# Optimization experiments

Measured on AMD Instinct MI355X. Metric: run time of the kernel, lower is better.

The kernel has to match this reference:

```python
import jax, jax.numpy as jnp
import numpy as np

EPS = 1e-5  # BatchNorm eps (torch default)

def setup_inputs() -> dict:
    key = jax.random.key(0)
    ks = jax.random.split(key, 24)
    B, NX, NY, F = 8, 128, 128, 128
    dims = [2 * F, 512, 256, 128, 64]
    d = {
        'x': jax.random.normal(ks[0], (B, NX, F), dtype=jnp.float32),
        'y': jax.random.normal(ks[1], (B, NY, F), dtype=jnp.float32),
    }
    i = 2
    for li, (din, dout) in enumerate(zip(dims[:-1], dims[1:]), start=1):
        d[f'w{li}'] = jax.random.normal(ks[i], (dout, din), dtype=jnp.float32) * (1.0 / np.sqrt(din)); i += 1
        d[f'b{li}'] = jax.random.normal(ks[i], (dout,), dtype=jnp.float32) * 0.02; i += 1
        if li < 4:  # BatchNorm1d on hidden layers only (eval mode: running stats)
            d[f'g{li}'] = 1.0 + 0.1 * jax.random.normal(ks[i], (dout,), dtype=jnp.float32); i += 1
            d[f'be{li}'] = 0.1 * jax.random.normal(ks[i], (dout,), dtype=jnp.float32); i += 1
            d[f'm{li}'] = 0.1 * jax.random.normal(ks[i], (dout,), dtype=jnp.float32); i += 1
            d[f'v{li}'] = 0.5 + jax.random.uniform(ks[i], (dout,), dtype=jnp.float32); i += 1
    return d

def _bn(h, g, be, m, v):
    # BatchNorm1d in eval mode over the channel (last) axis
    return (h - m) * (g * jax.lax.rsqrt(v + EPS)) + be

def reference(x, y,
              w1, b1, g1, be1, m1, v1,
              w2, b2, g2, be2, m2, v2,
              w3, b3, g3, be3, m3, v3,
              w4, b4):
    F = x.shape[-1]
    # First Linear on cat([x_i, y_j]) == split-weight broadcast add: avoids the
    # (B,nx,ny,2F) pairwise concat the torch code materializes (same math).
    wx, wy = w1[:, :F], w1[:, F:]                      # (512,F) each
    hx = jnp.einsum('bif,hf->bih', x, wx)              # (B,nx,512)
    hy = jnp.einsum('bjf,hf->bjh', y, wy)              # (B,ny,512)
    h = hx[:, :, None, :] + hy[:, None, :, :] + b1     # (B,nx,ny,512)
    h = jax.nn.relu(_bn(h, g1, be1, m1, v1))           # dropout is identity in eval
    h = jax.nn.relu(_bn(jnp.einsum('bijh,oh->bijo', h, w2) + b2, g2, be2, m2, v2))
    h = jax.nn.relu(_bn(jnp.einsum('bijh,oh->bijo', h, w3) + b3, g3, be3, m3, v3))
    e = jnp.einsum('bijh,oh->bijo', h, w4) + b4        # (B,nx,ny,64) embeddings
    # PSD path: einsum('bijk,bilk->bijl', e, e).sum(-1)
    #         == sum_k e[b,i,j,k] * (sum_l e[b,i,l,k])  -- avoids (B,nx,ny,ny)
    s = e.sum(axis=2)                                  # (B,nx,64)
    kernel = jnp.einsum('bijk,bik->bij', e, s)         # (B,nx,ny)
    return kernel
```

## Files before the change

### kernel.cpp

```cpp
#include <hip/hip_runtime.h>

#define EPS 1e-5f

typedef _Float16 half8 __attribute__((ext_vector_type(8)));
typedef _Float16 half4 __attribute__((ext_vector_type(4)));
typedef float f32x16 __attribute__((ext_vector_type(16)));
typedef float f32x4v __attribute__((ext_vector_type(4)));


__global__ __launch_bounds__(256)
void pre_kernel(
    const float* __restrict__ x, const float* __restrict__ y,
    const float* __restrict__ w1, const float* __restrict__ b1,
    const float* __restrict__ g1, const float* __restrict__ be1,
    const float* __restrict__ m1, const float* __restrict__ v1,
    const float* __restrict__ w2, const float* __restrict__ b2,
    const float* __restrict__ g2, const float* __restrict__ be2,
    const float* __restrict__ m2, const float* __restrict__ v2,
    const float* __restrict__ w3, const float* __restrict__ b3,
    const float* __restrict__ g3, const float* __restrict__ be3,
    const float* __restrict__ m3, const float* __restrict__ v3,
    const float* __restrict__ w4,
    _Float16* __restrict__ hxh, _Float16* __restrict__ hyh,
    _Float16* __restrict__ w2h, _Float16* __restrict__ w3h,
    _Float16* __restrict__ w4h,
    float* __restrict__ b2f, float* __restrict__ b3f)
{
    const int t = threadIdx.x;

    if (blockIdx.x >= 256) {
        int tid = (blockIdx.x - 256) * 256 + t;
        const int nth = 64 * 256;
        for (int idx = tid; idx < 256 * 512; idx += nth) {
            int n = idx >> 9, k = idx & 511;
            float a = g2[n] * rsqrtf(v2[n] + EPS);
            int addr = ((n >> 5) * 32 + (k >> 4)) * 512 + ((k >> 3) & 1) * 256 + (n & 31) * 8 + (k & 7);
            w2h[addr] = (_Float16)(a * w2[idx]);
        }
        for (int idx = tid; idx < 128 * 256; idx += nth) {
            int n = idx >> 8, k = idx & 255;
            float a = g3[n] * rsqrtf(v3[n] + EPS);
            int addr = ((n >> 5) * 16 + (k >> 4)) * 512 + ((k >> 3) & 1) * 256 + (n & 31) * 8 + (k & 7);
            w3h[addr] = (_Float16)(a * w3[idx]);
        }
        for (int idx = tid; idx < 64 * 128; idx += nth) {
            int n = idx >> 7, k = idx & 127;
            int addr = ((n >> 5) * 8 + (k >> 4)) * 512 + ((k >> 3) & 1) * 256 + (n & 31) * 8 + (k & 7);
            w4h[addr] = (_Float16)w4[idx];
        }
        if (tid < 256) {
            float a = g2[tid] * rsqrtf(v2[tid] + EPS);
            b2f[tid] = a * b2[tid] + be2[tid] - m2[tid] * a;
        } else if (tid < 384) {
            int n = tid - 256;
            float a = g3[n] * rsqrtf(v3[n] + EPS);
            b3f[n] = a * b3[n] + be3[n] - m3[n] * a;
        }
        return;
    }

    const int rg = blockIdx.x & 31;
    const int ng = (blockIdx.x >> 5) & 3;
    const int which = blockIdx.x >> 7;

    constexpr int LDA = 136;
    __shared__ _Float16 sh[32 * 136 + 128 * 136] __attribute__((aligned(16)));
    _Float16* xa = sh;
    _Float16* wb = sh + 32 * 136;

    const int rowbase = rg * 32;
    const float* src = which ? y : x;

#pragma unroll
    for (int p = 0; p < 4; ++p) {
        int c = p * 256 + t;
        int r = c >> 5, fo = (c & 31) * 4;
        f32x4v v = *(const f32x4v*)(src + (size_t)(rowbase + r) * 128 + fo);
        half4 h; h[0] = (_Float16)v[0]; h[1] = (_Float16)v[1];
        h[2] = (_Float16)v[2]; h[3] = (_Float16)v[3];
        *(half4*)(xa + r * LDA + fo) = h;
    }
#pragma unroll
    for (int p = 0; p < 16; ++p) {
        int c = p * 256 + t;
        int n = c >> 5, fo = (c & 31) * 4;
        f32x4v v = *(const f32x4v*)(w1 + (size_t)(ng * 128 + n) * 256 + which * 128 + fo);
        half4 h; h[0] = (_Float16)v[0]; h[1] = (_Float16)v[1];
        h[2] = (_Float16)v[2]; h[3] = (_Float16)v[3];
        *(half4*)(wb + n * LDA + fo) = h;
    }
    __syncthreads();

    const int wid = t >> 6;
    const int l = t & 63;
    const int l31 = l & 31, lh = l >> 5;

    f32x16 acc = (f32x16)0.f;
#pragma unroll
    for (int kc = 0; kc < 8; ++kc) {
        half8 af = *(const half8*)(xa + l31 * LDA + kc * 16 + lh * 8);
        half8 bf = *(const half8*)(wb + (wid * 32 + l31) * LDA + kc * 16 + lh * 8);
        acc = __builtin_amdgcn_mfma_f32_32x32x16_f16(af, bf, acc, 0, 0, 0);
    }

    const int n = ng * 128 + wid * 32 + l31;
    float alpha = g1[n] * rsqrtf(v1[n] + EPS);
    if (which == 0) {
        float bias = alpha * b1[n] + be1[n] - m1[n] * alpha;
#pragma unroll
        for (int r = 0; r < 16; ++r) {
            int m = (r & 3) + 8 * (r >> 2) + 4 * lh;
            hxh[(size_t)(rowbase + m) * 512 + n] = (_Float16)(alpha * acc[r] + bias);
        }
    } else {
        const int ks = n >> 4, lhh = (n >> 3) & 1, c = n & 7;
#pragma unroll
        for (int r = 0; r < 16; ++r) {
            int m = (r & 3) + 8 * (r >> 2) + 4 * lh;
            int R = rowbase + m;
            int bb = R >> 7, j = R & 127;
            int addr = bb * 65536 + ((j >> 5) * 32 + ks) * 512 + lhh * 256 + (j & 31) * 8 + c;
            hyh[addr] = (_Float16)(alpha * acc[r]);
        }
    }
}

__global__ __launch_bounds__(1024, 4)
void fused_kernel(
    const _Float16* __restrict__ hxh, const _Float16* __restrict__ hyh,
    const _Float16* __restrict__ w2h, const _Float16* __restrict__ w3h,
    const _Float16* __restrict__ w4h,
    const float* __restrict__ b2f, const float* __restrict__ b3f,
    const float* __restrict__ b4,
    float* __restrict__ out)
{
    constexpr int LD2 = 264;
    constexpr int LD3 = 136;
    constexpr int LDE = 68;

    __shared__ char smem[6400 + 67584] __attribute__((aligned(16)));
    _Float16* hxs = (_Float16*)smem;
    float* spart  = (float*)(smem + 2048);
    float* ss     = (float*)(smem + 6144);
    char* R1 = smem + 6400;
    _Float16* a2  = (_Float16*)R1;
    _Float16* a3  = (_Float16*)R1;
    float*    es  = (float*)R1;

    const int b  = blockIdx.x >> 6;
    const int ip = blockIdx.x & 63;
    const int i0 = ip * 2;
    const int t = threadIdx.x;
    const int wid = t >> 6;
    const int l   = t & 63;
    const int l31 = l & 31;
    const int lh  = l >> 5;

    if (t < 128) {
        int iv = t >> 6;
        *(half8*)(hxs + iv * 512 + (t & 63) * 8) =
            *(const half8*)(hxh + (size_t)(b * 128 + i0 + iv) * 512 + (t & 63) * 8);
    }
    __syncthreads();

    const int wm = wid >> 2, wn = wid & 3;

    const _Float16* pa  = hyh + (size_t)b * 65536 + (size_t)(wm * 32) * 512 + l * 8;
    const _Float16* pb0 = w2h + (size_t)(2 * wn) * 32 * 512 + l * 8;
    const _Float16* pb1 = pb0 + 32 * 512;

    const float bb0 = b2f[wn * 64 + l31];
    const float bb1 = b2f[wn * 64 + 32 + l31];
    f32x16 d0 = (f32x16)bb0, d1 = (f32x16)bb1;
    f32x16 e0 = (f32x16)bb0, e1 = (f32x16)bb1;

    half8 A0, B00, B01;
    half8 A1, B10, B11;

    auto LD0 = [&](int ks) {
        A0  = *(const half8*)(pa  + (size_t)ks * 512);
        B00 = *(const half8*)(pb0 + (size_t)ks * 512);
        B01 = *(const half8*)(pb1 + (size_t)ks * 512);
    };
    auto LD1 = [&](int ks) {
        A1  = *(const half8*)(pa  + (size_t)ks * 512);
        B10 = *(const half8*)(pb0 + (size_t)ks * 512);
        B11 = *(const half8*)(pb1 + (size_t)ks * 512);
    };
    auto RELU = [&](half8 a, half8 rx) {
        half8 s = a + rx;
        half8 af;
#pragma unroll
        for (int c = 0; c < 8; ++c)
            af[c] = s[c] > (_Float16)0.f ? s[c] : (_Float16)0.f;
        return af;
    };
    auto STEP0 = [&](int ks) {
        half8 rx0 = *(const half8*)(hxs + ks * 16 + lh * 8);
        half8 rx1 = *(const half8*)(hxs + 512 + ks * 16 + lh * 8);
        half8 af = RELU(A0, rx0);
        d0 = __builtin_amdgcn_mfma_f32_32x32x16_f16(af, B00, d0, 0, 0, 0);
        d1 = __builtin_amdgcn_mfma_f32_32x32x16_f16(af, B01, d1, 0, 0, 0);
        af = RELU(A0, rx1);
        e0 = __builtin_amdgcn_mfma_f32_32x32x16_f16(af, B00, e0, 0, 0, 0);
        e1 = __builtin_amdgcn_mfma_f32_32x32x16_f16(af, B01, e1, 0, 0, 0);
    };
    auto STEP1 = [&](int ks) {
        half8 rx0 = *(const half8*)(hxs + ks * 16 + lh * 8);
        half8 rx1 = *(const half8*)(hxs + 512 + ks * 16 + lh * 8);
        half8 af = RELU(A1, rx0);
        d0 = __builtin_amdgcn_mfma_f32_32x32x16_f16(af, B10, d0, 0, 0, 0);
        d1 = __builtin_amdgcn_mfma_f32_32x32x16_f16(af, B11, d1, 0, 0, 0);
        af = RELU(A1, rx1);
        e0 = __builtin_amdgcn_mfma_f32_32x32x16_f16(af, B10, e0, 0, 0, 0);
        e1 = __builtin_amdgcn_mfma_f32_32x32x16_f16(af, B11, e1, 0, 0, 0);
    };

    LD0(0);
#pragma unroll 2
    for (int ks = 0; ks < 32; ks += 2) {
        if (ks + 1 < 32) LD1(ks + 1);
        STEP0(ks);
        if (ks + 2 < 32) LD0(ks + 2);
        if (ks + 1 < 32) STEP1(ks + 1);
    }

    auto TAIL = [&](const f32x16& c0, const f32x16& c1, int iv) {
#pragma unroll
        for (int r = 0; r < 16; ++r) {
            int m = wm * 32 + (r & 3) + 8 * (r >> 2) + 4 * lh;
            a2[m * LD2 + wn * 64 + l31]      = (_Float16)fmaxf(c0[r], 0.f);
            a2[m * LD2 + wn * 64 + 32 + l31] = (_Float16)fmaxf(c1[r], 0.f);
        }
        __syncthreads();

        f32x16 g = (f32x16)(b3f[wn * 32 + l31]);
#pragma unroll 4
        for (int kc = 0; kc < 16; ++kc) {
            half8 bfr = *(const half8*)(w3h + (wn * 16 + kc) * 512 + l * 8);
            half8 af  = *(const half8*)(a2 + (wm * 32 + l31) * LD2 + kc * 16 + lh * 8);
            g = __builtin_amdgcn_mfma_f32_32x32x16_f16(af, bfr, g, 0, 0, 0);
        }
        __syncthreads();
#pragma unroll
        for (int r = 0; r < 16; ++r) {
            int m = wm * 32 + (r & 3) + 8 * (r >> 2) + 4 * lh;
            a3[m * LD3 + wn * 32 + l31] = (_Float16)fmaxf(g[r], 0.f);
        }
        __syncthreads();

        f32x16 acc4;
        const int wm4 = wid >> 1, wn4 = wid & 1;
        if (wid < 8) {
            acc4 = (f32x16)(b4[wn4 * 32 + l31]);
#pragma unroll
            for (int kc = 0; kc < 8; ++kc) {
                half8 afr = *(const half8*)(a3 + (wm4 * 32 + l31) * LD3 + kc * 16 + lh * 8);
                half8 bfr = *(const half8*)(w4h + (wn4 * 8 + kc) * 512 + l * 8);
                acc4 = __builtin_amdgcn_mfma_f32_32x32x16_f16(afr, bfr, acc4, 0, 0, 0);
            }
        }
        __syncthreads();
        if (wid < 8) {
#pragma unroll
            for (int r = 0; r < 16; ++r) {
                int m = wm4 * 32 + (r & 3) + 8 * (r >> 2) + 4 * lh;
                es[m * LDE + wn4 * 32 + l31] = acc4[r];
            }
        }
        __syncthreads();

        {
            float sv = 0.f;
#pragma unroll
            for (int jj = 0; jj < 8; ++jj) sv += es[(wid + jj * 16) * LDE + l];
            spart[wid * 64 + l] = sv;
        }
        __syncthreads();
        if (t < 64) {
            float s2 = 0.f;
#pragma unroll
            for (int r = 0; r < 16; ++r) s2 += spart[r * 64 + t];
            ss[t] = s2;
        }
        __syncthreads();
        {
            const int j = t >> 3, q = t & 7;
            float p = 0.f;
#pragma unroll
            for (int c = 0; c < 8; ++c) {
                int k = q + 8 * c;
                p += es[j * LDE + k] * ss[k];
            }
            p += __shfl_xor(p, 1);
            p += __shfl_xor(p, 2);
            p += __shfl_xor(p, 4);
            if (q == 0) out[(size_t)(b * 128 + iv) * 128 + j] = p;
        }
        __syncthreads();
    };

    TAIL(d0, d1, i0);
    TAIL(e0, e1, i0 + 1);
}

extern "C" void kernel_launch(void* const* d_in, const int* in_sizes, int n_in,
                              void* d_out, int out_size, void* d_ws, size_t ws_size,
                              hipStream_t stream)
{
    (void)in_sizes; (void)n_in; (void)out_size; (void)ws_size;

    const float* x   = (const float*)d_in[0];
    const float* y   = (const float*)d_in[1];
    const float* w1  = (const float*)d_in[2];
    const float* b1  = (const float*)d_in[3];
    const float* g1  = (const float*)d_in[4];
    const float* be1 = (const float*)d_in[5];
    const float* m1  = (const float*)d_in[6];
    const float* v1  = (const float*)d_in[7];
    const float* w2  = (const float*)d_in[8];
    const float* b2  = (const float*)d_in[9];
    const float* g2  = (const float*)d_in[10];
    const float* be2 = (const float*)d_in[11];
    const float* m2  = (const float*)d_in[12];
    const float* v2  = (const float*)d_in[13];
    const float* w3  = (const float*)d_in[14];
    const float* b3  = (const float*)d_in[15];
    const float* g3  = (const float*)d_in[16];
    const float* be3 = (const float*)d_in[17];
    const float* m3  = (const float*)d_in[18];
    const float* v3  = (const float*)d_in[19];
    const float* w4  = (const float*)d_in[20];
    const float* b4  = (const float*)d_in[21];
    float* out = (float*)d_out;

    float* b2f = (float*)d_ws;
    float* b3f = b2f + 256;
    _Float16* w2h = (_Float16*)(b3f + 128);
    _Float16* w3h = w2h + 131072;
    _Float16* w4h = w3h + 32768;
    _Float16* hxh = w4h + 8192;
    _Float16* hyh = hxh + 524288;

    hipLaunchKernelGGL(pre_kernel, dim3(320), dim3(256), 0, stream,
                       x, y, w1, b1, g1, be1, m1, v1,
                       w2, b2, g2, be2, m2, v2,
                       w3, b3, g3, be3, m3, v3,
                       w4,
                       hxh, hyh, w2h, w3h, w4h, b2f, b3f);

    hipLaunchKernelGGL(fused_kernel, dim3(512), dim3(1024), 0, stream,
                       hxh, hyh, w2h, w3h, w4h, b2f, b3f, b4, out);
}
```

Before: 73.29 us.

## Process both i-rows' tail concurrently with two 8-wave teams and double LDS regions

```diff
diff --git a/kernel.cpp b/kernel.cpp
--- a/kernel.cpp
+++ b/kernel.cpp
@@ -137,15 +137,13 @@
     constexpr int LD2 = 264;
     constexpr int LD3 = 136;
     constexpr int LDE = 68;
-
-    __shared__ char smem[6400 + 67584] __attribute__((aligned(16)));
+    constexpr int REG = 67584;
+
+    __shared__ char smem[8192 + 2 * REG] __attribute__((aligned(16)));
     _Float16* hxs = (_Float16*)smem;
     float* spart  = (float*)(smem + 2048);
     float* ss     = (float*)(smem + 6144);
-    char* R1 = smem + 6400;
-    _Float16* a2  = (_Float16*)R1;
-    _Float16* a3  = (_Float16*)R1;
-    float*    es  = (float*)R1;
+    char* R1 = smem + 8192;
 
     const int b  = blockIdx.x >> 6;
     const int ip = blockIdx.x & 63;
@@ -225,83 +223,99 @@
         if (ks + 1 < 32) STEP1(ks + 1);
     }
 
-    auto TAIL = [&](const f32x16& c0, const f32x16& c1, int iv) {
+    {
+        _Float16* a2_0 = (_Float16*)R1;
+        _Float16* a2_1 = (_Float16*)(R1 + REG);
 #pragma unroll
         for (int r = 0; r < 16; ++r) {
             int m = wm * 32 + (r & 3) + 8 * (r >> 2) + 4 * lh;
-            a2[m * LD2 + wn * 64 + l31]      = (_Float16)fmaxf(c0[r], 0.f);
-            a2[m * LD2 + wn * 64 + 32 + l31] = (_Float16)fmaxf(c1[r], 0.f);
-        }
-        __syncthreads();
-
-        f32x16 g = (f32x16)(b3f[wn * 32 + l31]);
+            a2_0[m * LD2 + wn * 64 + l31]      = (_Float16)fmaxf(d0[r], 0.f);
+            a2_0[m * LD2 + wn * 64 + 32 + l31] = (_Float16)fmaxf(d1[r], 0.f);
+            a2_1[m * LD2 + wn * 64 + l31]      = (_Float16)fmaxf(e0[r], 0.f);
+            a2_1[m * LD2 + wn * 64 + 32 + l31] = (_Float16)fmaxf(e1[r], 0.f);
+        }
+    }
+    __syncthreads();
+
+    const int team = wid >> 3;
+    const int tw   = wid & 7;
+    char* reg = R1 + team * REG;
+    _Float16* a2 = (_Float16*)reg;
+    _Float16* a3 = (_Float16*)reg;
+    float*    es = (float*)reg;
+    float* spart_t = spart + team * 512;
+    float* ss_t    = ss + team * 64;
+    const int iv = i0 + team;
+
+    const int wm3 = tw >> 2, wn3 = tw & 3;
+    f32x16 g0, g1;
+    {
+        float b3v = b3f[wn3 * 32 + l31];
+        g0 = (f32x16)b3v;
+        g1 = (f32x16)b3v;
+    }
 #pragma unroll 4
-        for (int kc = 0; kc < 16; ++kc) {
-            half8 bfr = *(const half8*)(w3h + (wn * 16 + kc) * 512 + l * 8);
-            half8 af  = *(const half8*)(a2 + (wm * 32 + l31) * LD2 + kc * 16 + lh * 8);
-            g = __builtin_amdgcn_mfma_f32_32x32x16_f16(af, bfr, g, 0, 0, 0);
-        }
-        __syncthreads();
+    for (int kc = 0; kc < 16; ++kc) {
+        half8 bfr = *(const half8*)(w3h + (wn3 * 16 + kc) * 512 + l * 8);
+        half8 af0 = *(const half8*)(a2 + (wm3 * 64 + l31) * LD2 + kc * 16 + lh * 8);
+        half8 af1 = *(const half8*)(a2 + (wm3 * 64 + 32 + l31) * LD2 + kc * 16 + lh * 8);
+        g0 = __builtin_amdgcn_mfma_f32_32x32x16_f16(af0, bfr, g0, 0, 0, 0);
+        g1 = __builtin_amdgcn_mfma_f32_32x32x16_f16(af1, bfr, g1, 0, 0, 0);
+    }
+    __syncthreads();
+#pragma unroll
+    for (int mt = 0; mt < 2; ++mt)
 #pragma unroll
         for (int r = 0; r < 16; ++r) {
-            int m = wm * 32 + (r & 3) + 8 * (r >> 2) + 4 * lh;
-            a3[m * LD3 + wn * 32 + l31] = (_Float16)fmaxf(g[r], 0.f);
-        }
-        __syncthreads();
-
-        f32x16 acc4;
-        const int wm4 = wid >> 1, wn4 = wid & 1;
-        if (wid < 8) {
-            acc4 = (f32x16)(b4[wn4 * 32 + l31]);
-#pragma unroll
-            for (int kc = 0; kc < 8; ++kc) {
-                half8 afr = *(const half8*)(a3 + (wm4 * 32 + l31) * LD3 + kc * 16 + lh * 8);
-                half8 bfr = *(const half8*)(w4h + (wn4 * 8 + kc) * 512 + l * 8);
-                acc4 = __builtin_amdgcn_mfma_f32_32x32x16_f16(afr, bfr, acc4, 0, 0, 0);
-            }
-        }
-        __syncthreads();
-        if (wid < 8) {
-#pragma unroll
-            for (int r = 0; r < 16; ++r) {
-                int m = wm4 * 32 + (r & 3) + 8 * (r >> 2) + 4 * lh;
-                es[m * LDE + wn4 * 32 + l31] = acc4[r];
-            }
-        }
-        __syncthreads();
-
-        {
-            float sv = 0.f;
-#pragma unroll
-            for (int jj = 0; jj < 8; ++jj) sv += es[(wid + jj * 16) * LDE + l];
-            spart[wid * 64 + l] = sv;
-        }
-        __syncthreads();
-        if (t < 64) {
-            float s2 = 0.f;
-#pragma unroll
-            for (int r = 0; r < 16; ++r) s2 += spart[r * 64 + t];
-            ss[t] = s2;
-        }
-        __syncthreads();
-        {
-            const int j = t >> 3, q = t & 7;
-            float p = 0.f;
-#pragma unroll
-            for (int c = 0; c < 8; ++c) {
-                int k = q + 8 * c;
-                p += es[j * LDE + k] * ss[k];
-            }
-            p += __shfl_xor(p, 1);
-            p += __shfl_xor(p, 2);
-            p += __shfl_xor(p, 4);
-            if (q == 0) out[(size_t)(b * 128 + iv) * 128 + j] = p;
-        }
-        __syncthreads();
-    };
-
-    TAIL(d0, d1, i0);
-    TAIL(e0, e1, i0 + 1);
+            int m = wm3 * 64 + mt * 32 + (r & 3) + 8 * (r >> 2) + 4 * lh;
+            a3[m * LD3 + wn3 * 32 + l31] = (_Float16)fmaxf(mt ? g1[r] : g0[r], 0.f);
+        }
+    __syncthreads();
+
+    const int wm4 = tw >> 1, wn4 = tw & 1;
+    f32x16 acc4 = (f32x16)(b4[wn4 * 32 + l31]);
+#pragma unroll
+    for (int kc = 0; kc < 8; ++kc) {
+        half8 afr = *(const half8*)(a3 + (wm4 * 32 + l31) * LD3 + kc * 16 + lh * 8);
+        half8 bfr = *(const half8*)(w4h + (wn4 * 8 + kc) * 512 + l * 8);
+        acc4 = __builtin_amdgcn_mfma_f32_32x32x16_f16(afr, bfr, acc4, 0, 0, 0);
+    }
+    __syncthreads();
+#pragma unroll
+    for (int r = 0; r < 16; ++r) {
+        int m = wm4 * 32 + (r & 3) + 8 * (r >> 2) + 4 * lh;
+        es[m * LDE + wn4 * 32 + l31] = acc4[r];
+    }
+    __syncthreads();
+
+    {
+        float sv = 0.f;
+#pragma unroll
+        for (int jj = 0; jj < 16; ++jj) sv += es[(tw + jj * 8) * LDE + l];
+        spart_t[tw * 64 + l] = sv;
+    }
+    __syncthreads();
+    if ((t & 511) < 64) {
+        int tt = t & 63;
+        float s2 = 0.f;
+#pragma unroll
+        for (int r = 0; r < 8; ++r) s2 += spart_t[r * 64 + tt];
+        ss_t[tt] = s2;
+    }
+    __syncthreads();
+    {
+        const int tt = t & 511;
+        const int j = tt >> 2, q = tt & 3;
+        float p = 0.f;
+#pragma unroll
+        for (int c = 0; c < 16; ++c) {
+            int k = q + 4 * c;
+            p += es[j * LDE + k] * ss_t[k];
+        }
+        p += __shfl_xor(p, 1);
+        p += __shfl_xor(p, 2);
+        if (q == 0) out[(size_t)(b * 128 + iv) * 128 + j] = p;
+    }
 }
 
 extern "C" void kernel_launch(void* const* d_in, const int* in_sizes, int n_in,
```

Result: faster. 68.45 us (-6.6%).
